# Kernel tuning notes

Measured on AMD Instinct MI355X. Metric: run time of the kernel, lower is better.

## Reference

```python
import jax, jax.numpy as jnp
import numpy as np

B, T, F, C = 1024, 64, 1024, 3  # batch, num_trees, num_features, num_of_cls
NSLOT, N2 = 5, 16


def setup_inputs() -> dict:
    key = jax.random.key(0)
    ks = jax.random.split(key, 9)
    return {
        "d": jax.random.normal(ks[0], (B, 2048), jnp.float32),
        "idx": jax.random.randint(ks[1], (T, F), 0, 2048, jnp.int32),
        "cc": jax.random.randint(ks[2], (T, C), 0, NSLOT, jnp.int32),
        "w_clc": jax.random.normal(ks[3], (T, F, 2), jnp.float32) * 0.02,
        "b_clc": jax.random.normal(ks[4], (T, 2), jnp.float32) * 0.02,
        "w1": jax.random.normal(ks[5], (T, F, C), jnp.float32) * 0.02,
        "b1": jax.random.normal(ks[6], (T, C), jnp.float32) * 0.02,
        "w2": jax.random.normal(ks[7], (T, F + C, N2), jnp.float32) * 0.02,
        "b2": jax.random.normal(ks[8], (T, N2), jnp.float32) * 0.02,
    }


def reference(d, idx, cc, w_clc, b_clc, w1, b1, w2, b2):
    # Per-tree random feature gather: [B, T, F]
    g = d[:, idx]
    # Gate: clc[i](d[:, idx[i]]).log_softmax(-1)
    w = jax.nn.log_softmax(jnp.einsum('btf,tfc->btc', g, w_clc) + b_clc, axis=-1)
    # AgentCLS (eval mode: dropout = identity)
    logits1 = jnp.einsum('btf,tfc->btc', g, w1) + b1          # [B,T,C]
    y1 = jax.nn.log_softmax(logits1, axis=-1)
    x2 = jnp.concatenate([g, jax.nn.relu(logits1)], axis=-1)  # [B,T,F+C]
    y2 = jax.nn.log_softmax(jnp.einsum('btf,tfc->btc', x2, w2) + b2, axis=-1)
    # Gate-weighted scatter combine (get_output math)
    gate = jnp.exp(w[..., 1:2])                               # [B,T,1]
    onehot = jax.nn.one_hot(cc, NSLOT, dtype=d.dtype)         # [T,C,5]
    out5 = jnp.einsum('btc,tcx->bx', jnp.exp(y1) * gate, onehot)
    count5 = jnp.einsum('bt,tx->bx', gate[..., 0], onehot.sum(1))
    out5 = jnp.where(count5 > 0, out5 / jnp.where(count5 > 0, count5, 1.0), 0.0)
    gsum = gate.sum(1)                                        # [B,1]
    out16 = (jnp.exp(y2) * gate).sum(1) / gsum
    return jnp.concatenate([out5, out16], axis=-1)            # [B,21]
```

## Files before the change

kernel.cpp:

```cpp
#include <hip/hip_runtime.h>

#define NT 64
#define NF 1024
#define NB 1024
#define ND 2048
#define NTP 32
#define NN2 (NT * NTP)
#define NP 27
#define NW2ROW 1027
#define BK 64
#define BM 64
#define BN 64

typedef __attribute__((ext_vector_type(8))) short short8;
typedef __attribute__((ext_vector_type(4))) float f32x4;

static __device__ __forceinline__ unsigned short f2bf(float x) {
    unsigned u = __float_as_uint(x);
    unsigned r = (u + 0x7FFFu + ((u >> 16) & 1u)) >> 16;
    return (unsigned short)r;
}

__global__ __launch_bounds__(1024) void prep_kernel(
    const int* __restrict__ idx, const float* __restrict__ w_clc,
    const float* __restrict__ w1, const float* __restrict__ w2,
    const float* __restrict__ d, unsigned short* __restrict__ Wf,
    unsigned short* __restrict__ db)
{
    __shared__ __align__(16) float tile[6 * ND];
    int bid = blockIdx.x;
    int tid = threadIdx.x;

    if (bid < 256) {
        int t = bid >> 2, kq = bid & 3;
        int kw    = (kq == 0) ? 6 : 5;
        int kbase = (kq == 0) ? 0 : 1 + 5 * kq;

        float4* tz = (float4*)tile;
        for (int i = tid; i < 6 * ND / 4; i += 1024) tz[i] = make_float4(0, 0, 0, 0);
        __syncthreads();

        {
            int f = tid;
            int j = idx[t * NF + f];
            const float* w2row = &w2[((size_t)t * NW2ROW + f) * 16];
            float v[6];
            if (kq == 0) {
                float2 a = *(const float2*)&w_clc[(size_t)(t * NF + f) * 2];
                const float* p1 = &w1[(size_t)(t * NF + f) * 3];
                v[0] = a.x; v[1] = a.y;
                v[2] = p1[0]; v[3] = p1[1]; v[4] = p1[2];
                v[5] = w2row[0];
            } else {
                int c0 = 5 * kq - 4;
#pragma unroll
                for (int c = 0; c < 5; ++c) v[c] = w2row[c0 + c];
                v[5] = 0.f;
            }
#pragma unroll
            for (int c = 0; c < 6; ++c)
                if (c < kw) atomicAdd(&tile[c * ND + j], v[c]);
        }
        __syncthreads();

        for (int i = tid; i < kw * 256; i += 1024) {
            int c = i >> 8, col8 = (i & 255) * 8;
            const float* tr = &tile[c * ND + col8];
            union { unsigned short u[8]; uint4 v; } pk;
#pragma unroll
            for (int e = 0; e < 8; ++e) pk.u[e] = f2bf(tr[e]);
            *(uint4*)&Wf[(size_t)(t * NTP + kbase + c) * ND + col8] = pk.v;
        }
        int padbase = (kq == 0) ? 21 : 20 + 3 * kq;
        int npad    = (kq == 0) ? 2 : 3;
        uint4 z = make_uint4(0, 0, 0, 0);
        for (int i = tid; i < npad * 256; i += 1024) {
            int c = i >> 8, col8 = (i & 255) * 8;
            *(uint4*)&Wf[(size_t)(t * NTP + padbase + c) * ND + col8] = z;
        }
    } else {
        int cb = bid - 256;
        int i16 = (cb * 1024 + tid) * 16;
#pragma unroll
        for (int h = 0; h < 2; ++h) {
            int i8 = i16 + h * 8;
            float4 a = *(const float4*)&d[i8];
            float4 b = *(const float4*)&d[i8 + 4];
            union { unsigned short u[8]; uint4 v; } pk;
            pk.u[0] = f2bf(a.x); pk.u[1] = f2bf(a.y); pk.u[2] = f2bf(a.z); pk.u[3] = f2bf(a.w);
            pk.u[4] = f2bf(b.x); pk.u[5] = f2bf(b.y); pk.u[6] = f2bf(b.z); pk.u[7] = f2bf(b.w);
            *(uint4*)&db[i8] = pk.v;
        }
    }
}

__global__ __launch_bounds__(256, 2) void fused_kernel(
    const unsigned short* __restrict__ A,
    const unsigned short* __restrict__ Bm,
    const float* __restrict__ b_clc, const float* __restrict__ b1,
    const float* __restrict__ b2, const float* __restrict__ w2,
    const int* __restrict__ cc, float* __restrict__ ptl2)
{
    __shared__ __align__(16) char smem[32768];
    unsigned short (*As)[BM][BK] = (unsigned short(*)[BM][BK])smem;
    unsigned short (*Bs)[BN][BK] = (unsigned short(*)[BN][BK])(smem + 16384);
    float* Cl  = (float*)smem;
    float* red = (float*)(smem + 16896);

    int tid = threadIdx.x;
    int lane = tid & 63;
    int wv = tid >> 6;
    int wr = wv & 1;
    int wq = wv >> 1;
    int nb = blockIdx.x;
    int mb = blockIdx.y;
    int m0 = mb * BM;
    int n0 = nb * BN;
    int r0 = lane & 15;
    int kq = lane >> 4;
    int sx = r0 & 7;
    int sl0 = ((0 * 4 + kq) ^ sx) * 8;
    int sl1 = ((1 * 4 + kq) ^ sx) * 8;

    f32x4 acc[2][2];
#pragma unroll
    for (int mi = 0; mi < 2; ++mi)
#pragma unroll
        for (int ni = 0; ni < 2; ++ni) acc[mi][ni] = (f32x4)0.f;

#define STAGE(buf, kt)                                                          \
    {                                                                           \
        size_t koff = (size_t)(kt) * BK;                                        \
        _Pragma("unroll")                                                       \
        for (int p = 0; p < 2; ++p) {                                           \
            int chunk = p * 256 + tid;                                          \
            int row = chunk >> 3, c = chunk & 7;                                \
            int csw = (c ^ (row & 7)) * 8;                                      \
            const unsigned short* ga = A + (size_t)(m0 + row) * ND + koff + csw;\
            __builtin_amdgcn_global_load_lds(                                   \
                (const __attribute__((address_space(1))) void*)ga,              \
                (__attribute__((address_space(3))) void*)&As[buf][row][c * 8],  \
                16, 0, 0);                                                      \
        }                                                                       \
        _Pragma("unroll")                                                       \
        for (int p = 0; p < 2; ++p) {                                           \
            int chunk = p * 256 + tid;                                          \
            int row = chunk >> 3, c = chunk & 7;                                \
            int csw = (c ^ (row & 7)) * 8;                                      \
            const unsigned short* gb = Bm + (size_t)(n0 + row) * ND + koff + csw;\
            __builtin_amdgcn_global_load_lds(                                   \
                (const __attribute__((address_space(1))) void*)gb,              \
                (__attribute__((address_space(3))) void*)&Bs[buf][row][c * 8],  \
                16, 0, 0);                                                      \
        }                                                                       \
    }

    STAGE(0, 0);
    __syncthreads();

    int cur = 0;
    for (int kt = 0; kt < 32; ++kt) {
        if (kt < 31) STAGE(cur ^ 1, kt + 1);

        short8 af[2][2], bf[2][2];
#pragma unroll
        for (int mi = 0; mi < 2; ++mi) {
            af[mi][0] = *(const short8*)&As[cur][wr*32 + mi*16 + r0][sl0];
            af[mi][1] = *(const short8*)&As[cur][wr*32 + mi*16 + r0][sl1];
        }
#pragma unroll
        for (int ni = 0; ni < 2; ++ni) {
            bf[ni][0] = *(const short8*)&Bs[cur][wq*32 + ni*16 + r0][sl0];
            bf[ni][1] = *(const short8*)&Bs[cur][wq*32 + ni*16 + r0][sl1];
        }
#pragma unroll
        for (int ks = 0; ks < 2; ++ks)
#pragma unroll
            for (int mi = 0; mi < 2; ++mi)
#pragma unroll
                for (int ni = 0; ni < 2; ++ni)
                    acc[mi][ni] = __builtin_amdgcn_mfma_f32_16x16x32_bf16(
                        af[mi][ks], bf[ni][ks], acc[mi][ni], 0, 0, 0);
        __syncthreads();
        cur ^= 1;
    }
#undef STAGE

#pragma unroll
    for (int mi = 0; mi < 2; ++mi)
#pragma unroll
        for (int ni = 0; ni < 2; ++ni) {
            int n = wq * 32 + ni * 16 + r0;
            int bl = wr * 32 + mi * 16 + kq * 4;
#pragma unroll
            for (int q = 0; q < 4; ++q)
                Cl[(bl + q) * 65 + n] = acc[mi][ni][q];
        }
    __syncthreads();

    int tl = tid >> 6;
    int bl = lane;
    float s[NP];
#pragma unroll
    for (int k = 0; k < NP; ++k) s[k] = 0.f;

    if (tl < 2) {
        int t = nb * 2 + tl;

        float a21[21];
#pragma unroll
        for (int k = 0; k < 21; ++k) a21[k] = Cl[bl * 65 + tl * 32 + k];

        float L0 = a21[0] + b_clc[t * 2 + 0];
        float L1 = a21[1] + b_clc[t * 2 + 1];
        float mm = fmaxf(L0, L1);
        float e0 = __expf(L0 - mm), e1 = __expf(L1 - mm);
        float gate = e1 / (e0 + e1);

        float l1v[3];
        float m1 = -3.0e38f;
#pragma unroll
        for (int c = 0; c < 3; ++c) {
            l1v[c] = a21[2 + c] + b1[t * 3 + c];
            m1 = fmaxf(m1, l1v[c]);
        }
        float p1[3]; float S1 = 0.f;
#pragma unroll
        for (int c = 0; c < 3; ++c) { p1[c] = __expf(l1v[c] - m1); S1 += p1[c]; }
        float invS1g = gate / S1;

        float r0f = fmaxf(l1v[0], 0.f);
        float r1f = fmaxf(l1v[1], 0.f);
        float r2f = fmaxf(l1v[2], 0.f);

        const float* w2t = w2 + ((size_t)t * NW2ROW + NF) * 16;
        float l2[16]; float m2 = -3.0e38f;
#pragma unroll
        for (int nn = 0; nn < 16; ++nn) {
            float v = a21[5 + nn] + b2[t * 16 + nn];
            v = fmaf(r0f, w2t[nn], v);
            v = fmaf(r1f, w2t[16 + nn], v);
            v = fmaf(r2f, w2t[32 + nn], v);
            l2[nn] = v;
            m2 = fmaxf(m2, v);
        }
        float S2 = 0.f; float p2[16];
#pragma unroll
        for (int nn = 0; nn < 16; ++nn) { p2[nn] = __expf(l2[nn] - m2); S2 += p2[nn]; }
        float invS2g = gate * __frcp_rn(S2);

#pragma unroll
        for (int c = 0; c < 3; ++c) {
            int sl = cc[t * 3 + c];
            float pc = p1[c] * invS1g;
#pragma unroll
            for (int x = 0; x < 5; ++x) {
                if (sl == x) { s[x] += pc; s[5 + x] += gate; }
            }
        }
#pragma unroll
        for (int nn = 0; nn < 16; ++nn) s[10 + nn] += p2[nn] * invS2g;
        s[26] += gate;
    }

    if (tl == 1) {
#pragma unroll
        for (int k = 0; k < NP; ++k) red[k * 64 + bl] = s[k];
    }
    __syncthreads();
    if (tl != 0) return;

#pragma unroll
    for (int k = 0; k < NP; ++k) s[k] += red[k * 64 + bl];

    float* pt = ptl2 + (size_t)nb * NP * NB + m0 + bl;
#pragma unroll
    for (int k = 0; k < NP; ++k)
        pt[(size_t)k * NB] = s[k];
}

__global__ __launch_bounds__(1024) void finalize_kernel(
    const float* __restrict__ ptl2, float* __restrict__ out)
{
    __shared__ float red[8][NP][64];
    int lane = threadIdx.x & 63;
    int w = threadIdx.x >> 6;
    int b = blockIdx.x * 64 + lane;

    float s[NP];
#pragma unroll
    for (int k = 0; k < NP; ++k) s[k] = 0.f;
#pragma unroll
    for (int i = 0; i < 2; ++i) {
        const float* pt = ptl2 + (size_t)(w * 2 + i) * NP * NB + b;
#pragma unroll
        for (int k = 0; k < NP; ++k) s[k] += pt[(size_t)k * NB];
    }

    if (w >= 8) {
#pragma unroll
        for (int k = 0; k < NP; ++k) red[w - 8][k][lane] = s[k];
    }
    __syncthreads();
    if (w < 8) {
#pragma unroll
        for (int k = 0; k < NP; ++k) s[k] += red[w][k][lane];
    }
    __syncthreads();
    if (w >= 4 && w < 8) {
#pragma unroll
        for (int k = 0; k < NP; ++k) red[w - 4][k][lane] = s[k];
    }
    __syncthreads();
    if (w < 4) {
#pragma unroll
        for (int k = 0; k < NP; ++k) s[k] += red[w][k][lane];
    }
    __syncthreads();
    if (w >= 2 && w < 4) {
#pragma unroll
        for (int k = 0; k < NP; ++k) red[w - 2][k][lane] = s[k];
    }
    __syncthreads();
    if (w < 2) {
#pragma unroll
        for (int k = 0; k < NP; ++k) s[k] += red[w][k][lane];
    }
    __syncthreads();
    if (w == 1) {
#pragma unroll
        for (int k = 0; k < NP; ++k) red[0][k][lane] = s[k];
    }
    __syncthreads();
    if (w != 0) return;
#pragma unroll
    for (int k = 0; k < NP; ++k) s[k] += red[0][k][lane];

    float* ob = out + (size_t)b * 21;
#pragma unroll
    for (int x = 0; x < 5; ++x) {
        float c = s[5 + x];
        ob[x] = (c > 0.f) ? (s[x] / c) : 0.f;
    }
    float invg = 1.f / s[26];
#pragma unroll
    for (int n = 0; n < 16; ++n) ob[5 + n] = s[10 + n] * invg;
}

extern "C" void kernel_launch(void* const* d_in, const int* in_sizes, int n_in,
                              void* d_out, int out_size, void* d_ws, size_t ws_size,
                              hipStream_t stream)
{
    const float* d     = (const float*)d_in[0];
    const int*   idx   = (const int*)  d_in[1];
    const int*   cc    = (const int*)  d_in[2];
    const float* w_clc = (const float*)d_in[3];
    const float* b_clc = (const float*)d_in[4];
    const float* w1    = (const float*)d_in[5];
    const float* b1    = (const float*)d_in[6];
    const float* w2    = (const float*)d_in[7];
    const float* b2    = (const float*)d_in[8];
    float* out = (float*)d_out;

    unsigned short* Wf = (unsigned short*)d_ws;
    unsigned short* db = Wf + (size_t)NN2 * ND;
    float* ptl2 = (float*)(db + (size_t)NB * ND);

    prep_kernel<<<384, 1024, 0, stream>>>(idx, w_clc, w1, w2, d, Wf, db);
    fused_kernel<<<dim3(32, 16), 256, 0, stream>>>(db, Wf, b_clc, b1, b2, w2, cc, ptl2);
    finalize_kernel<<<16, 1024, 0, stream>>>(ptl2, out);
}
```

Baseline: 44.02 us.

## Split weight scatter by destination column range instead of output channel groups

```diff
diff --git a/kernel.cpp b/kernel.cpp
--- a/kernel.cpp
+++ b/kernel.cpp
@@ -27,59 +27,69 @@
     const float* __restrict__ d, unsigned short* __restrict__ Wf,
     unsigned short* __restrict__ db)
 {
-    __shared__ __align__(16) float tile[6 * ND];
+    __shared__ __align__(16) float tile[21 * 256];
     int bid = blockIdx.x;
     int tid = threadIdx.x;
 
-    if (bid < 256) {
-        int t = bid >> 2, kq = bid & 3;
-        int kw    = (kq == 0) ? 6 : 5;
-        int kbase = (kq == 0) ? 0 : 1 + 5 * kq;
+    if (bid < 512) {
+        int t = bid >> 3, je = bid & 7;
 
         float4* tz = (float4*)tile;
-        for (int i = tid; i < 6 * ND / 4; i += 1024) tz[i] = make_float4(0, 0, 0, 0);
+        for (int i = tid; i < 1344; i += 1024) tz[i] = make_float4(0, 0, 0, 0);
         __syncthreads();
 
         {
             int f = tid;
             int j = idx[t * NF + f];
-            const float* w2row = &w2[((size_t)t * NW2ROW + f) * 16];
-            float v[6];
-            if (kq == 0) {
+            if ((j >> 8) == je) {
+                int jl = j & 255;
                 float2 a = *(const float2*)&w_clc[(size_t)(t * NF + f) * 2];
+                atomicAdd(&tile[0 * 256 + jl], a.x);
+                atomicAdd(&tile[1 * 256 + jl], a.y);
                 const float* p1 = &w1[(size_t)(t * NF + f) * 3];
-                v[0] = a.x; v[1] = a.y;
-                v[2] = p1[0]; v[3] = p1[1]; v[4] = p1[2];
-                v[5] = w2row[0];
-            } else {
-                int c0 = 5 * kq - 4;
-#pragma unroll
-                for (int c = 0; c < 5; ++c) v[c] = w2row[c0 + c];
-                v[5] = 0.f;
+                atomicAdd(&tile[2 * 256 + jl], p1[0]);
+                atomicAdd(&tile[3 * 256 + jl], p1[1]);
+                atomicAdd(&tile[4 * 256 + jl], p1[2]);
+                const float* w2row = &w2[((size_t)t * NW2ROW + f) * 16];
+                float4 q0 = *(const float4*)&w2row[0];
+                float4 q1 = *(const float4*)&w2row[4];
+                float4 q2 = *(const float4*)&w2row[8];
+                float4 q3 = *(const float4*)&w2row[12];
+                atomicAdd(&tile[ 5 * 256 + jl], q0.x);
+                atomicAdd(&tile[ 6 * 256 + jl], q0.y);
+                atomicAdd(&tile[ 7 * 256 + jl], q0.z);
+                atomicAdd(&tile[ 8 * 256 + jl], q0.w);
+                atomicAdd(&tile[ 9 * 256 + jl], q1.x);
+                atomicAdd(&tile[10 * 256 + jl], q1.y);
+                atomicAdd(&tile[11 * 256 + jl], q1.z);
+                atomicAdd(&tile[12 * 256 + jl], q1.w);
+                atomicAdd(&tile[13 * 256 + jl], q2.x);
+                atomicAdd(&tile[14 * 256 + jl], q2.y);
+                atomicAdd(&tile[15 * 256 + jl], q2.z);
+                atomicAdd(&tile[16 * 256 + jl], q2.w);
+                atomicAdd(&tile[17 * 256 + jl], q3.x);
+                atomicAdd(&tile[18 * 256 + jl], q3.y);
+                atomicAdd(&tile[19 * 256 + jl], q3.z);
+                atomicAdd(&tile[20 * 256 + jl], q3.w);
             }
-#pragma unroll
-            for (int c = 0; c < 6; ++c)
-                if (c < kw) atomicAdd(&tile[c * ND + j], v[c]);
         }
         __syncthreads();
 
-        for (int i = tid; i < kw * 256; i += 1024) {
-            int c = i >> 8, col8 = (i & 255) * 8;
-            const float* tr = &tile[c * ND + col8];
+        for (int i = tid; i < 672; i += 1024) {
+            int c = i >> 5, off = (i & 31) * 8;
+            const float* tr = &tile[c * 256 + off];
             union { unsigned short u[8]; uint4 v; } pk;
 #pragma unroll
             for (int e = 0; e < 8; ++e) pk.u[e] = f2bf(tr[e]);
-            *(uint4*)&Wf[(size_t)(t * NTP + kbase + c) * ND + col8] = pk.v;
-        }
-        int padbase = (kq == 0) ? 21 : 20 + 3 * kq;
-        int npad    = (kq == 0) ? 2 : 3;
+            *(uint4*)&Wf[(size_t)(t * NTP + c) * ND + je * 256 + off] = pk.v;
+        }
         uint4 z = make_uint4(0, 0, 0, 0);
-        for (int i = tid; i < npad * 256; i += 1024) {
-            int c = i >> 8, col8 = (i & 255) * 8;
-            *(uint4*)&Wf[(size_t)(t * NTP + padbase + c) * ND + col8] = z;
+        for (int i = tid; i < 352; i += 1024) {
+            int c = 21 + (i >> 5), off = (i & 31) * 8;
+            *(uint4*)&Wf[(size_t)(t * NTP + c) * ND + je * 256 + off] = z;
         }
     } else {
-        int cb = bid - 256;
+        int cb = bid - 512;
         int i16 = (cb * 1024 + tid) * 16;
 #pragma unroll
         for (int h = 0; h < 2; ++h) {
@@ -366,7 +376,7 @@
     unsigned short* db = Wf + (size_t)NN2 * ND;
     float* ptl2 = (float*)(db + (size_t)NB * ND);
 
-    prep_kernel<<<384, 1024, 0, stream>>>(idx, w_clc, w1, w2, d, Wf, db);
+    prep_kernel<<<640, 1024, 0, stream>>>(idx, w_clc, w1, w2, d, Wf, db);
     fused_kernel<<<dim3(32, 16), 256, 0, stream>>>(db, Wf, b_clc, b1, b2, w2, cc, ptl2);
     finalize_kernel<<<16, 1024, 0, stream>>>(ptl2, out);
 }
```

Result: faster. 42.93 us (-2.5%).
